# Kernel optimization log

Hardware: AMD Instinct MI355X
Metric: run time of the kernel (lower is better)

Reference implementation:

```python
import jax, jax.numpy as jnp
import numpy as np

N = 50000          # nodes
E = 1_600_000      # edges (avg degree 32)
F_IN = 256
F_OUT = 256
ALPHA = 0.2        # LeakyReLU negative slope


def setup_inputs() -> dict:
    key = jax.random.key(0)
    ks = jax.random.split(key, 7)
    x = jax.random.normal(ks[0], (N, F_IN), dtype=jnp.float32)
    row = jax.random.randint(ks[1], (E,), 0, N, dtype=jnp.int32)  # dst i
    col = jax.random.randint(ks[2], (E,), 0, N, dtype=jnp.int32)  # src j
    W_w = jax.random.normal(ks[3], (F_IN, F_OUT), dtype=jnp.float32) / np.sqrt(F_IN).astype(np.float32)
    W_b = jax.random.normal(ks[4], (F_OUT,), dtype=jnp.float32) * 0.01
    a_w = jax.random.normal(ks[5], (2 * F_OUT,), dtype=jnp.float32) / np.sqrt(2 * F_OUT).astype(np.float32)
    a_b = jax.random.normal(ks[6], (1,), dtype=jnp.float32) * 0.01
    return {"x": x, "W_w": W_w, "W_b": W_b, "a_w": a_w, "a_b": a_b,
            "row": row, "col": col}


def reference(x, W_w, W_b, a_w, a_b, row, col):
    # Wh = W(x): [N, F_OUT]
    Wh = x @ W_w + W_b
    # e[i,j] = leakyrelu(a1 . Wh[j] + a2 . Wh[i] + b)
    # (repeat puts Wh[j] in the first half of the concat, repeat_interleave Wh[i] in the second)
    f_dst_part = Wh @ a_w[:F_OUT]   # contribution of column node j
    f_row_part = Wh @ a_w[F_OUT:]   # contribution of row node i
    e = f_dst_part[col] + f_row_part[row] + a_b[0]          # [E]
    e = jnp.where(e > 0, e, ALPHA * e)                      # LeakyReLU
    # sparse softmax over dim=1 (segment = row i), adjacency values are 1.0
    m = jax.ops.segment_max(e, row, num_segments=N)         # [N]
    ex = jnp.exp(e - m[row])
    denom = jax.ops.segment_sum(ex, row, num_segments=N)    # [N]
    att = ex / denom[row]                                   # [E]
    # h'[i] = sum_j att[i,j] * Wh[j]  (spmm), empty rows stay zero
    h_prime = jax.ops.segment_sum(att[:, None] * Wh[col], row, num_segments=N)
    return jax.nn.relu(h_prime)
```

## Files before the change

kernel.cpp:

```cpp
#include <hip/hip_runtime.h>
#include <math.h>

#define N_NODES 50000
#define N_EDGES 1600000
#define F 256
#define ALPHA 0.2f
#define NP 50048
#define NB 196
#define CAP 10240
#define EPB 4096
#define NAB ((N_EDGES + EPB - 1) / EPB)
#define UNROLL 16
#define GEMM_BLOCKS 782
#define FVEC_SLOTS 2048

typedef short bf16x8 __attribute__((ext_vector_type(8)));
typedef float f32x4 __attribute__((ext_vector_type(4)));
typedef _Float16 half4 __attribute__((ext_vector_type(4)));

__device__ __forceinline__ unsigned short f2bf(float f) {
  union { float f; unsigned u; } v; v.f = f;
  unsigned u = v.u;
  return (unsigned short)((u + 0x7fffu + ((u >> 16) & 1u)) >> 16);
}

__device__ __forceinline__ unsigned short f2h_bits(float f) {
  union { _Float16 h; unsigned short u; } v;
  v.h = (_Float16)f;
  return v.u;
}

__device__ __forceinline__ float h_bits2f(unsigned short u) {
  union { _Float16 h; unsigned short u; } v;
  v.u = u;
  return (float)v.h;
}

__global__ __launch_bounds__(256) void prep_w(const float* __restrict__ W,
                                              const float* __restrict__ a_w,
                                              const float* __restrict__ W_b,
                                              const float* __restrict__ a_b,
                                              unsigned short* __restrict__ Wt,
                                              float* __restrict__ wa,
                                              float* __restrict__ cb,
                                              int* __restrict__ gcur) {
  if (blockIdx.x == 64) {
    if (threadIdx.x < NB) gcur[threadIdx.x] = 0;
    return;
  }
  const int lane = threadIdx.x & 63, w = threadIdx.x >> 6;
  const int k = blockIdx.x * 4 + w;
  float4 wv = *(const float4*)(W + (size_t)k * F + lane * 4);
  float4 a1 = *(const float4*)(a_w + lane * 4);
  float4 a2 = *(const float4*)(a_w + F + lane * 4);
  Wt[(size_t)(lane * 4 + 0) * F + k] = f2bf(wv.x);
  Wt[(size_t)(lane * 4 + 1) * F + k] = f2bf(wv.y);
  Wt[(size_t)(lane * 4 + 2) * F + k] = f2bf(wv.z);
  Wt[(size_t)(lane * 4 + 3) * F + k] = f2bf(wv.w);
  float s1 = wv.x * a1.x + wv.y * a1.y + wv.z * a1.z + wv.w * a1.w;
  float s2 = wv.x * a2.x + wv.y * a2.y + wv.z * a2.z + wv.w * a2.w;
#pragma unroll
  for (int off = 32; off > 0; off >>= 1) {
    s1 += __shfl_down(s1, off, 64);
    s2 += __shfl_down(s2, off, 64);
  }
  if (lane == 0) { wa[k] = s1; wa[F + k] = s2; }
  if (blockIdx.x == 0 && w == 0) {
    float4 b = *(const float4*)(W_b + lane * 4);
    float t1 = b.x * (a1.x + a2.x) + b.y * (a1.y + a2.y) +
               b.z * (a1.z + a2.z) + b.w * (a1.w + a2.w);
#pragma unroll
    for (int off = 32; off > 0; off >>= 1) t1 += __shfl_down(t1, off, 64);
    if (lane == 0) cb[0] = t1 + a_b[0];
  }
}

#define LDSK 72
__global__ __launch_bounds__(256) void gemm_fvec_binA2(
    const float* __restrict__ x,
    const unsigned short* __restrict__ Wt,
    const float* __restrict__ bias,
    const float* __restrict__ wa,
    const int* __restrict__ row,
    const int* __restrict__ col,
    _Float16* __restrict__ Wh,
    float* __restrict__ f_dst,
    float* __restrict__ f_row,
    int* __restrict__ gcur,
    unsigned* __restrict__ gstage) {
  __shared__ char smem[2 * 128 * LDSK * 2];
  if (blockIdx.x < GEMM_BLOCKS) {
    short* As = (short*)smem;
    short* Bs = As + 128 * LDSK;
    const int tid = threadIdx.x;
    const int lane = tid & 63;
    const int w = tid >> 6;
    const int wm = w >> 1, wn = w & 1;
    const int m0 = (blockIdx.x >> 1) * 128;
    const int n0 = (blockIdx.x & 1) * 128;
    f32x4 acc[4][4] = {{{0.f, 0.f, 0.f, 0.f}}};
    const int srow = tid >> 3;
    const int schunk = tid & 7;
    for (int k0 = 0; k0 < F; k0 += 64) {
#pragma unroll
      for (int i = 0; i < 4; ++i) {
        int r = i * 32 + srow;
        int gm = m0 + r; if (gm > N_NODES - 1) gm = N_NODES - 1;
        const float* src = x + (size_t)gm * F + k0 + schunk * 8;
        float4 lo = *(const float4*)src;
        float4 hi = *(const float4*)(src + 4);
        bf16x8 v;
        v[0] = (short)f2bf(lo.x); v[1] = (short)f2bf(lo.y);
        v[2] = (short)f2bf(lo.z); v[3] = (short)f2bf(lo.w);
        v[4] = (short)f2bf(hi.x); v[5] = (short)f2bf(hi.y);
        v[6] = (short)f2bf(hi.z); v[7] = (short)f2bf(hi.w);
        *(bf16x8*)&As[r * LDSK + schunk * 8] = v;
        *(bf16x8*)&Bs[r * LDSK + schunk * 8] =
            *(const bf16x8*)(Wt + (size_t)(n0 + r) * F + k0 + schunk * 8);
      }
      __syncthreads();
#pragma unroll
      for (int kk = 0; kk < 64; kk += 32) {
        const int rowsel = lane & 15;
        const int ksel = kk + (lane >> 4) * 8;
        bf16x8 af[4], bfr[4];
#pragma unroll
        for (int t = 0; t < 4; ++t) {
          af[t] = *(bf16x8*)&As[(wm * 64 + t * 16 + rowsel) * LDSK + ksel];
          bfr[t] = *(bf16x8*)&Bs[(wn * 64 + t * 16 + rowsel) * LDSK + ksel];
        }
#pragma unroll
        for (int mi = 0; mi < 4; ++mi)
#pragma unroll
          for (int nj = 0; nj < 4; ++nj)
            acc[mi][nj] = __builtin_amdgcn_mfma_f32_16x16x32_bf16(
                af[mi], bfr[nj], acc[mi][nj], 0, 0, 0);
      }
      __syncthreads();
    }
    const int crow = (lane >> 4) * 4;
    const int ccol = lane & 15;
#pragma unroll
    for (int nj = 0; nj < 4; ++nj) {
      int gc = n0 + wn * 64 + nj * 16 + ccol;
      float bv = bias[gc];
#pragma unroll
      for (int mi = 0; mi < 4; ++mi) {
        int gr = m0 + wm * 64 + mi * 16 + crow;
#pragma unroll
        for (int r = 0; r < 4; ++r)
          Wh[(size_t)(gr + r) * F + gc] = (_Float16)(acc[mi][nj][r] + bv);
      }
    }
    return;
  }
  if (blockIdx.x < GEMM_BLOCKS + NAB) {
    int* h = (int*)smem;
    int* lofs = h + NB;
    int* lcur = lofs + NB;
    int* gb = lcur + NB;
    unsigned* stage = (unsigned*)(gb + NB);
    const int t = threadIdx.x;
    for (int i = t; i < NB; i += 256) { h[i] = 0; lcur[i] = 0; }
    __syncthreads();
    const int base = (blockIdx.x - GEMM_BLOCKS) * EPB;
    const int cnt = min(EPB, N_EDGES - base);
#pragma unroll
    for (int j = 0; j < 16; ++j) {
      int k = base + j * 256 + t;
      if (k < N_EDGES) atomicAdd(&h[row[k] >> 8], 1);
    }
    __syncthreads();
    if (t == 0) {
      int run = 0;
      for (int i = 0; i < NB; ++i) { lofs[i] = run; run += h[i]; }
    }
    __syncthreads();
    if (t < NB && h[t] > 0) gb[t] = atomicAdd(&gcur[t], h[t]);
    __syncthreads();
#pragma unroll
    for (int j = 0; j < 16; ++j) {
      int k = base + j * 256 + t;
      if (k < N_EDGES) {
        int r = row[k], b = r >> 8;
        int lp = lofs[b] + atomicAdd(&lcur[b], 1);
        stage[lp] = ((unsigned)b << 24) | ((unsigned)(r & 255) << 16) |
                    (unsigned)col[k];
      }
    }
    __syncthreads();
#pragma unroll
    for (int j = 0; j < 16; ++j) {
      int s = j * 256 + t;
      if (s < cnt) {
        unsigned wv = stage[s];
        int b = wv >> 24;
        gstage[(size_t)b * CAP + gb[b] + (s - lofs[b])] = wv & 0x00FFFFFFu;
      }
    }
    return;
  }
  const int lane = threadIdx.x & 63, w = threadIdx.x >> 6;
  const int slot = blockIdx.x - GEMM_BLOCKS - NAB;
  float4 v1 = *(const float4*)(wa + lane * 4);
  float4 v2 = *(const float4*)(wa + F + lane * 4);
  for (int node = slot * 4 + w; node < N_NODES; node += FVEC_SLOTS * 4) {
    float4 xv = *(const float4*)(x + (size_t)node * F + lane * 4);
    float s1 = xv.x * v1.x + xv.y * v1.y + xv.z * v1.z + xv.w * v1.w;
    float s2 = xv.x * v2.x + xv.y * v2.y + xv.z * v2.z + xv.w * v2.w;
#pragma unroll
    for (int off = 32; off > 0; off >>= 1) {
      s1 += __shfl_down(s1, off, 64);
      s2 += __shfl_down(s2, off, 64);
    }
    if (lane == 0) { f_dst[node] = s1; f_row[node] = s2; }
  }
}

__global__ __launch_bounds__(512) void binB(const int* __restrict__ gcur,
                                            const unsigned* __restrict__ gstage,
                                            const float* __restrict__ f_dst,
                                            const float* __restrict__ f_row,
                                            const float* __restrict__ cb,
                                            int2* __restrict__ rsc,
                                            float* __restrict__ inv_denom,
                                            unsigned* __restrict__ csr) {
  __shared__ int cnt2[2048];
  __shared__ int cur2[2048];
  __shared__ int rcnt[256], rbase[256];
  __shared__ float dsum[256];
  const int t = threadIdx.x;
  const int b = blockIdx.x;
  for (int i = t; i < 2048; i += 512) cnt2[i] = 0;
  if (t < 256) dsum[t] = 0.f;
  __syncthreads();
  const int nb = gcur[b];
  const int start = b * CAP;
  const float cbs = cb[0];
  for (int s = t; s < nb; s += 512) {
    unsigned wv = gstage[start + s];
    int key = (((wv >> 16) & 255) << 3) | ((wv & 0xFFFFu) >> 13);
    atomicAdd(&cnt2[key], 1);
  }
  __syncthreads();
  if (t < 256) {
    int tot = 0;
#pragma unroll
    for (int q = 0; q < 8; ++q) tot += cnt2[t * 8 + q];
    rcnt[t] = tot;
  }
  __syncthreads();
  if (t == 0) {
    int run = 0;
    for (int i = 0; i < 256; ++i) { rbase[i] = run; run += rcnt[i]; }
  }
  __syncthreads();
  if (t < 256) {
    int base = start + rbase[t];
    int g = (b << 8) + t;
    if (g < N_NODES) rsc[g] = make_int2(base, rcnt[t]);
    int run = base;
#pragma unroll
    for (int q = 0; q < 8; ++q) { cur2[t * 8 + q] = run; run += cnt2[t * 8 + q]; }
  }
  __syncthreads();
  for (int s = t; s < nb; s += 512) {
    unsigned wv = gstage[start + s];
    int lr = (wv >> 16) & 255;
    int c = wv & 0xFFFF;
    float ev = f_dst[c] + f_row[(b << 8) + lr] + cbs;
    ev = ev > 0.f ? ev : ALPHA * ev;
    float ex = __expf(ev);
    int p = atomicAdd(&cur2[(lr << 3) | (c >> 13)], 1);
    csr[p] = ((unsigned)f2h_bits(ex) << 16) | (unsigned)c;
    atomicAdd(&dsum[lr], ex);
  }
  __syncthreads();
  if (t < 256) {
    int g = (b << 8) + t;
    if (g < N_NODES) inv_denom[g] = (rcnt[t] > 0) ? (1.0f / dsum[t]) : 0.f;
  }
}

__global__ __launch_bounds__(256) void gat_pull(const int2* __restrict__ rsc,
                                                const unsigned* __restrict__ csr,
                                                const float* __restrict__ inv_denom,
                                                const _Float16* __restrict__ Wh,
                                                float* __restrict__ out) {
  const int lane = threadIdx.x & 63, w = threadIdx.x >> 6;
  const int i = blockIdx.x * 4 + w;
  if (i >= N_NODES) return;
  const int2 rc = rsc[i];
  const int s = rc.x, e = rc.x + rc.y;
  const char* whb = (const char*)Wh;
  const unsigned laneoff = (unsigned)lane * 8u;
  float4 acc = make_float4(0.f, 0.f, 0.f, 0.f);
  for (int p = s; p < e; p += UNROLL) {
    unsigned wv[UNROLL];
#pragma unroll
    for (int j = 0; j < UNROLL; ++j) {
      int q = p + j;
      wv[j] = csr[q < e ? q : s];
    }
    half4 v[UNROLL];
#pragma unroll
    for (int j = 0; j < UNROLL; ++j) {
      unsigned off = (wv[j] & 0xFFFFu) * 512u + laneoff;
      v[j] = *(const half4*)(whb + off);
    }
#pragma unroll
    for (int j = 0; j < UNROLL; ++j) {
      float xw = h_bits2f((unsigned short)(wv[j] >> 16));
      xw = (p + j < e) ? xw : 0.f;
      acc.x += xw * (float)v[j][0];
      acc.y += xw * (float)v[j][1];
      acc.z += xw * (float)v[j][2];
      acc.w += xw * (float)v[j][3];
    }
  }
  const float inv = inv_denom[i];
  acc.x = fmaxf(acc.x * inv, 0.f); acc.y = fmaxf(acc.y * inv, 0.f);
  acc.z = fmaxf(acc.z * inv, 0.f); acc.w = fmaxf(acc.w * inv, 0.f);
  ((float4*)out)[(size_t)i * 64 + lane] = acc;
}

extern "C" void kernel_launch(void* const* d_in, const int* in_sizes, int n_in,
                              void* d_out, int out_size, void* d_ws, size_t ws_size,
                              hipStream_t stream) {
  const float* x   = (const float*)d_in[0];
  const float* W_w = (const float*)d_in[1];
  const float* W_b = (const float*)d_in[2];
  const float* a_w = (const float*)d_in[3];
  const float* a_b = (const float*)d_in[4];
  const int*   row = (const int*)d_in[5];
  const int*   col = (const int*)d_in[6];
  float* out = (float*)d_out;

  float* ws = (float*)d_ws;
  size_t off = 0;
  _Float16* Wh = (_Float16*)(ws + off); off += (size_t)NP * F / 2;
  unsigned short* Wt = (unsigned short*)(ws + off); off += (F * F) / 2;
  float* wa = ws + off;            off += 2 * F;
  float* cb = ws + off;            off += 8;
  float* f_dst = ws + off;         off += NP;
  float* f_row = ws + off;         off += NP;
  int* gcur = (int*)(ws + off);    off += NB;
  int2* rsc = (int2*)(ws + off);   off += 2 * (size_t)NP;
  float* inv_denom = (float*)(ws + off); off += NP;
  unsigned* gstage = (unsigned*)(ws + off); off += (size_t)NB * CAP;
  unsigned* csr = (unsigned*)(ws + off); off += (size_t)NB * CAP;
  (void)ws_size; (void)in_sizes; (void)n_in; (void)out_size;

  hipLaunchKernelGGL(prep_w, dim3(65), dim3(256), 0, stream, W_w, a_w, W_b,
                     a_b, Wt, wa, cb, gcur);
  hipLaunchKernelGGL(gemm_fvec_binA2, dim3(GEMM_BLOCKS + NAB + FVEC_SLOTS),
                     dim3(256), 0, stream, x, Wt, W_b, wa, row, col, Wh,
                     f_dst, f_row, gcur, gstage);
  hipLaunchKernelGGL(binB, dim3(NB), dim3(512), 0, stream, gcur, gstage,
                     f_dst, f_row, cb, rsc, inv_denom, csr);
  hipLaunchKernelGGL(gat_pull, dim3((N_NODES + 3) / 4), dim3(256), 0, stream,
                     rsc, csr, inv_denom, Wh, out);
}
```

Baseline: 283.6 us.

## Split wavefront into two half-waves processing edges in parallel with 16-byte gathers

The pull kernel now has each half of a wavefront handle alternate edges, each lane loading 8 fp16 channels (16 bytes) per gathered row instead of 4. The two halves are combined with a cross-half shuffle, and waves grid-stride over nodes using a fixed block count. The aim is wider memory transactions and more independent gathers in flight per wave. In exchange it adds shuffle and select overhead, and the remainder loop handles tails in steps of 4 edges.

```diff
diff --git a/kernel.cpp b/kernel.cpp
--- a/kernel.cpp
+++ b/kernel.cpp
@@ -10,13 +10,14 @@
 #define CAP 10240
 #define EPB 4096
 #define NAB ((N_EDGES + EPB - 1) / EPB)
-#define UNROLL 16
 #define GEMM_BLOCKS 782
 #define FVEC_SLOTS 2048
+#define PULL_BLOCKS 2048
 
 typedef short bf16x8 __attribute__((ext_vector_type(8)));
 typedef float f32x4 __attribute__((ext_vector_type(4)));
 typedef _Float16 half4 __attribute__((ext_vector_type(4)));
+typedef _Float16 half8 __attribute__((ext_vector_type(8)));
 
 __device__ __forceinline__ unsigned short f2bf(float f) {
   union { float f; unsigned u; } v; v.f = f;
@@ -287,41 +288,61 @@
                                                 const float* __restrict__ inv_denom,
                                                 const _Float16* __restrict__ Wh,
                                                 float* __restrict__ out) {
-  const int lane = threadIdx.x & 63, w = threadIdx.x >> 6;
-  const int i = blockIdx.x * 4 + w;
-  if (i >= N_NODES) return;
-  const int2 rc = rsc[i];
-  const int s = rc.x, e = rc.x + rc.y;
+  const int lane = threadIdx.x & 63;
+  const int eo = lane >> 5;
+  const int l32 = lane & 31;
+  const int wid = blockIdx.x * 4 + (threadIdx.x >> 6);
+  const int nw = PULL_BLOCKS * 4;
   const char* whb = (const char*)Wh;
-  const unsigned laneoff = (unsigned)lane * 8u;
-  float4 acc = make_float4(0.f, 0.f, 0.f, 0.f);
-  for (int p = s; p < e; p += UNROLL) {
-    unsigned wv[UNROLL];
-#pragma unroll
-    for (int j = 0; j < UNROLL; ++j) {
-      int q = p + j;
-      wv[j] = csr[q < e ? q : s];
-    }
-    half4 v[UNROLL];
-#pragma unroll
-    for (int j = 0; j < UNROLL; ++j) {
-      unsigned off = (wv[j] & 0xFFFFu) * 512u + laneoff;
-      v[j] = *(const half4*)(whb + off);
-    }
-#pragma unroll
-    for (int j = 0; j < UNROLL; ++j) {
-      float xw = h_bits2f((unsigned short)(wv[j] >> 16));
-      xw = (p + j < e) ? xw : 0.f;
-      acc.x += xw * (float)v[j][0];
-      acc.y += xw * (float)v[j][1];
-      acc.z += xw * (float)v[j][2];
-      acc.w += xw * (float)v[j][3];
-    }
-  }
-  const float inv = inv_denom[i];
-  acc.x = fmaxf(acc.x * inv, 0.f); acc.y = fmaxf(acc.y * inv, 0.f);
-  acc.z = fmaxf(acc.z * inv, 0.f); acc.w = fmaxf(acc.w * inv, 0.f);
-  ((float4*)out)[(size_t)i * 64 + lane] = acc;
+  const unsigned chanoff = (unsigned)l32 * 16u;
+  for (int i = wid; i < N_NODES; i += nw) {
+    const int2 rc = rsc[i];
+    const int s = rc.x, e = rc.x + rc.y;
+    float acc[8] = {0.f, 0.f, 0.f, 0.f, 0.f, 0.f, 0.f, 0.f};
+    int p = s;
+    for (; p + 16 <= e; p += 16) {
+      unsigned wv[8];
+#pragma unroll
+      for (int j = 0; j < 8; ++j) wv[j] = csr[p + 2 * j + eo];
+      half8 v[8];
+#pragma unroll
+      for (int j = 0; j < 8; ++j) {
+        unsigned off = (wv[j] & 0xFFFFu) * 512u + chanoff;
+        v[j] = *(const half8*)(whb + off);
+      }
+#pragma unroll
+      for (int j = 0; j < 8; ++j) {
+        float xw = h_bits2f((unsigned short)(wv[j] >> 16));
+#pragma unroll
+        for (int c = 0; c < 8; ++c) acc[c] += xw * (float)v[j][c];
+      }
+    }
+    for (; p < e; p += 4) {
+      int q0 = p + eo, q1 = p + 2 + eo;
+      unsigned w0 = csr[q0 < e ? q0 : s];
+      unsigned w1 = csr[q1 < e ? q1 : s];
+      unsigned off0 = (w0 & 0xFFFFu) * 512u + chanoff;
+      unsigned off1 = (w1 & 0xFFFFu) * 512u + chanoff;
+      half8 v0 = *(const half8*)(whb + off0);
+      half8 v1 = *(const half8*)(whb + off1);
+      float xw0 = (q0 < e) ? h_bits2f((unsigned short)(w0 >> 16)) : 0.f;
+      float xw1 = (q1 < e) ? h_bits2f((unsigned short)(w1 >> 16)) : 0.f;
+#pragma unroll
+      for (int c = 0; c < 8; ++c) acc[c] += xw0 * (float)v0[c];
+#pragma unroll
+      for (int c = 0; c < 8; ++c) acc[c] += xw1 * (float)v1[c];
+    }
+#pragma unroll
+    for (int c = 0; c < 8; ++c) acc[c] += __shfl_xor(acc[c], 32, 64);
+    const float inv = inv_denom[i];
+    float r0 = eo ? acc[4] : acc[0];
+    float r1 = eo ? acc[5] : acc[1];
+    float r2 = eo ? acc[6] : acc[2];
+    float r3 = eo ? acc[7] : acc[3];
+    float4 o = make_float4(fmaxf(r0 * inv, 0.f), fmaxf(r1 * inv, 0.f),
+                           fmaxf(r2 * inv, 0.f), fmaxf(r3 * inv, 0.f));
+    ((float4*)out)[(size_t)i * 64 + l32 * 2 + eo] = o;
+  }
 }
 
 extern "C" void kernel_launch(void* const* d_in, const int* in_sizes, int n_in,
@@ -358,6 +379,6 @@
                      f_dst, f_row, gcur, gstage);
   hipLaunchKernelGGL(binB, dim3(NB), dim3(512), 0, stream, gcur, gstage,
                      f_dst, f_row, cb, rsc, inv_denom, csr);
-  hipLaunchKernelGGL(gat_pull, dim3((N_NODES + 3) / 4), dim3(256), 0, stream,
+  hipLaunchKernelGGL(gat_pull, dim3(PULL_BLOCKS), dim3(256), 0, stream,
                      rsc, csr, inv_denom, Wh, out);
 }
```

Result: no change. 285.0 us (+0.5%).
